# Performance work log

Hardware: AMD Instinct MI355X
Metric: run time of the kernel (lower is better)

Reference implementation:

```python
import jax, jax.numpy as jnp
import numpy as np

RADIUS = 0.1
NSAMPLE = 32


def ball_query_cnt(radius, nsample, xyz, new_xyz):
    """xyz: (B,N,3), new_xyz: (B,npoint,3) -> cnt (B,npoint) int32, idx (B,npoint,nsample) int32.
    Matches pointnet2 CUDA semantics: first `nsample` in-radius points in index order;
    unfilled slots replicate the first found index (0 if none found)."""
    N = xyz.shape[1]
    # (B, npoint, N) squared distances
    d2 = jnp.sum((new_xyz[:, :, None, :] - xyz[:, None, :, :]) ** 2, axis=-1)
    mask = d2 < radius * radius
    pos = jnp.arange(N, dtype=jnp.int32)
    # key encodes position so that top_k returns the LOWEST valid positions first
    key = jnp.where(mask, N - pos, -N)
    topk_vals, _ = jax.lax.top_k(key, nsample)          # (B, npoint, nsample)
    valid = topk_vals > 0
    idx = (N - topk_vals).astype(jnp.int32)
    first = jnp.where(valid[..., :1], idx[..., :1], 0)   # fill value per query
    idx = jnp.where(valid, idx, first)
    cnt = jnp.minimum(mask.sum(axis=-1), nsample).astype(jnp.int32)
    return cnt, idx


def group(features, idx):
    """features: (B,C,N), idx: (B,npoint,nsample) -> (B,C,npoint,nsample)."""
    return jax.vmap(lambda f, i: f[:, i])(features, idx)


def setup_inputs() -> dict:
    key = jax.random.key(0)
    k1, k2, k3 = jax.random.split(key, 3)
    B, N, npoint, C = 4, 16384, 2048, 64
    xyz = jax.random.uniform(k1, (B, N, 3), dtype=jnp.float32)
    new_xyz = jax.random.uniform(k2, (B, npoint, 3), dtype=jnp.float32)
    features = jax.random.normal(k3, (B, C, N), dtype=jnp.float32)
    return {"xyz": xyz, "new_xyz": new_xyz, "features": features}


def reference(xyz, new_xyz, features):
    idx_cnt, idx = ball_query_cnt(RADIUS, NSAMPLE, xyz, new_xyz)
    xyz_t = jnp.transpose(xyz, (0, 2, 1))                      # (B,3,N)
    grouped_xyz = group(xyz_t, idx)                            # (B,3,npoint,nsample)
    grouped_xyz = grouped_xyz - jnp.transpose(new_xyz, (0, 2, 1))[..., None]
    grouped_features = group(features, idx)                    # (B,C,npoint,nsample)
    new_features = jnp.concatenate([grouped_xyz, grouped_features], axis=1)
    return idx_cnt, new_features
```

## Files before the change

### kernel.cpp

```cpp
#include <hip/hip_runtime.h>

#define B        4
#define N        16384
#define NPOINT   2048
#define C        64
#define NSAMPLE  32
#define CH       (C + 3)
#define RADIUS2  0.01f
#define NCELL    1000
#define CSTRIDE  1032
#define CAP      256

#define WAVE_FENCE() asm volatile("s_waitcnt lgkmcnt(0)" ::: "memory")

__device__ __forceinline__ int clamp10(int v) {
    return v < 0 ? 0 : (v > 9 ? 9 : v);
}

__device__ __forceinline__ int cell_of(float x, float y, float z) {
    return (clamp10((int)(x * 10.f)) * 10 + clamp10((int)(y * 10.f))) * 10
         + clamp10((int)(z * 10.f));
}

__global__ __launch_bounds__(256) void zero_kernel(int* __restrict__ p, int n) {
    const int i = blockIdx.x * 256 + threadIdx.x;
    if (i < n) p[i] = 0;
}

__device__ __forceinline__ void transpose_body(const float* __restrict__ f,
                                               float* __restrict__ ft,
                                               int n0, int b, int t,
                                               float (*tile)[65]) {
    const int r16 = t >> 4;
    const int x4  = t & 15;
    #pragma unroll
    for (int it = 0; it < 4; ++it) {
        const int cc = it * 16 + r16;
        const float4 v = *(const float4*)(f + ((size_t)b * C + cc) * N + n0 + x4 * 4);
        tile[cc][x4 * 4 + 0] = v.x;
        tile[cc][x4 * 4 + 1] = v.y;
        tile[cc][x4 * 4 + 2] = v.z;
        tile[cc][x4 * 4 + 3] = v.w;
    }
    __syncthreads();
    #pragma unroll
    for (int it = 0; it < 4; ++it) {
        const int nn = it * 16 + r16;
        float4 v;
        v.x = tile[x4 * 4 + 0][nn];
        v.y = tile[x4 * 4 + 1][nn];
        v.z = tile[x4 * 4 + 2][nn];
        v.w = tile[x4 * 4 + 3][nn];
        *(float4*)(ft + ((size_t)b * N + n0 + nn) * C + x4 * 4) = v;
    }
}

__global__ __launch_bounds__(256) void prep_kernel(const float* __restrict__ xyz,
                                                   int* __restrict__ cnt,
                                                   const float* __restrict__ f,
                                                   float* __restrict__ ft) {
    __shared__ float tile[64][65];
    if (blockIdx.x < (B * N / 256)) {
        const int g = blockIdx.x * 256 + threadIdx.x;
        const int b = g >> 14;
        const float x = xyz[g * 3 + 0], y = xyz[g * 3 + 1], z = xyz[g * 3 + 2];
        atomicAdd(&cnt[(b << 10) + cell_of(x, y, z)], 1);
    } else {
        const int bi = blockIdx.x - (B * N / 256);
        transpose_body(f, ft, (bi & 255) * 64, bi >> 8, threadIdx.x, tile);
    }
}

__global__ __launch_bounds__(256) void feat_transpose_kernel(
    const float* __restrict__ f, float* __restrict__ ft) {
    __shared__ float tile[64][65];
    transpose_body(f, ft, blockIdx.x * 64, blockIdx.y, threadIdx.x, tile);
}

__global__ __launch_bounds__(1024) void prefix_kernel(int* __restrict__ cnt,
                                                      int* __restrict__ cs) {
    __shared__ int wsum[16];
    const int t = threadIdx.x, b = blockIdx.x;
    const int w = t >> 6, l = t & 63;
    const int v = (t < NCELL) ? cnt[(b << 10) + t] : 0;
    int inc = v;
    #pragma unroll
    for (int off = 1; off < 64; off <<= 1) {
        const int u = __shfl_up(inc, off);
        if (l >= off) inc += u;
    }
    if (l == 63) wsum[w] = inc;
    __syncthreads();
    if (t < 16) {
        int s = wsum[t];
        #pragma unroll
        for (int off = 1; off < 16; off <<= 1) {
            const int u = __shfl_up(s, off, 16);
            if (t >= off) s += u;
        }
        wsum[t] = s;
    }
    __syncthreads();
    const int base = (w > 0) ? wsum[w - 1] : 0;
    const int excl = base + inc - v;
    if (t <= NCELL) cs[b * CSTRIDE + t] = excl;
    if (t < NCELL)  cnt[(b << 10) + t] = excl;
}

__global__ __launch_bounds__(256) void scatter_kernel(const float* __restrict__ xyz,
                                                      int* __restrict__ cursor,
                                                      float4* __restrict__ sp) {
    const int g = blockIdx.x * 256 + threadIdx.x;
    const int b = g >> 14;
    const int n = g & (N - 1);
    const float x = xyz[g * 3 + 0], y = xyz[g * 3 + 1], z = xyz[g * 3 + 2];
    const int pos = atomicAdd(&cursor[(b << 10) + cell_of(x, y, z)], 1);
    sp[(b << 14) + pos] = make_float4(x, y, z, __int_as_float(n));
}

__global__ __launch_bounds__(256, 6) void qg_fused_kernel(
    const float*  __restrict__ xyz,
    const float*  __restrict__ new_xyz,
    const float*  __restrict__ ft,
    const int*    __restrict__ cs,
    const float4* __restrict__ sp,
    float* __restrict__ out_cnt,
    float* __restrict__ out_feat)
{
    const int w = threadIdx.x >> 6;
    const int l = threadIdx.x & 63;
    const int q = blockIdx.x * 4 + w;
    const int b = q >> 11;
    const int j = q & (NPOINT - 1);

    __shared__ int   cand_s[4][CAP];
    __shared__ int   si_s[4][NSAMPLE];
    __shared__ float tile_s[4][35 * 33];
    int*   cand = cand_s[w];
    int*   s_i  = si_s[w];
    float* tile = tile_s[w];

    const float qx = new_xyz[q * 3 + 0];
    const float qy = new_xyz[q * 3 + 1];
    const float qz = new_xyz[q * 3 + 2];

    const int cx = clamp10((int)(qx * 10.f));
    const int cy = clamp10((int)(qy * 10.f));
    const int cz = clamp10((int)(qz * 10.f));
    const int z0 = cz > 0 ? cz - 1 : 0;
    const int z1 = cz < 9 ? cz + 1 : 9;

    int sv = 0, ev = 0;
    if (l < 9) {
        const int xx = cx - 1 + l / 3;
        const int yy = cy - 1 + l % 3;
        if (xx >= 0 && xx <= 9 && yy >= 0 && yy <= 9) {
            const int cb = (xx * 10 + yy) * 10;
            sv = cs[b * CSTRIDE + cb + z0];
            ev = cs[b * CSTRIDE + cb + z1 + 1];
        }
    }
    int rs[9], re[9];
    #pragma unroll
    for (int r = 0; r < 9; ++r) {
        rs[r] = __shfl(sv, r);
        re[r] = __shfl(ev, r);
    }

    const unsigned long long ltmask = (1ull << l) - 1ull;
    const float4* spb = sp + ((size_t)b << 14);

    float4 pt[9];
    bool   a[9];
    #pragma unroll
    for (int r = 0; r < 9; ++r) {
        const int p = rs[r] + l;
        a[r] = p < re[r];
        pt[r] = a[r] ? spb[p] : make_float4(1e9f, 1e9f, 1e9f, 0.f);
    }
    int total = 0, ncand = 0;
    #pragma unroll
    for (int r = 0; r < 9; ++r) {
        const float dx = pt[r].x - qx, dy = pt[r].y - qy, dz = pt[r].z - qz;
        const float d2 = dx * dx + dy * dy + dz * dz;
        const bool in = a[r] && (d2 < RADIUS2);
        const unsigned long long m = __ballot(in);
        if (in) {
            const int slot = ncand + __popcll(m & ltmask);
            if (slot < CAP) cand[slot] = __float_as_int(pt[r].w);
        }
        const int c = __popcll(m);
        total += c;
        ncand = ncand + c > CAP ? CAP : ncand + c;
    }
    #pragma unroll 1
    for (int r = 0; r < 9; ++r) {
        #pragma unroll 1
        for (int p0 = rs[r] + 64; p0 < re[r]; p0 += 64) {
            const int p = p0 + l;
            const bool act = p < re[r];
            float4 pv = make_float4(1e9f, 1e9f, 1e9f, 0.f);
            if (act) pv = spb[p];
            const float dx = pv.x - qx, dy = pv.y - qy, dz = pv.z - qz;
            const float d2 = dx * dx + dy * dy + dz * dz;
            const bool in = act && (d2 < RADIUS2);
            const unsigned long long m = __ballot(in);
            if (in) {
                const int slot = ncand + __popcll(m & ltmask);
                if (slot < CAP) cand[slot] = __float_as_int(pv.w);
            }
            const int c = __popcll(m);
            total += c;
            ncand = ncand + c > CAP ? CAP : ncand + c;
        }
    }
    WAVE_FENCE();

    int cntv;
    if (total > CAP) {
        const float* xb = xyz + (size_t)b * N * 3;
        int cnt2 = 0;
        for (int base = 0; base < N; base += 64) {
            const int p = base + l;
            const float dx = xb[p * 3 + 0] - qx;
            const float dy = xb[p * 3 + 1] - qy;
            const float dz = xb[p * 3 + 2] - qz;
            const float d2 = dx * dx + dy * dy + dz * dz;
            const bool in = d2 < RADIUS2;
            const unsigned long long m = __ballot(in);
            if (in) {
                const int slot = cnt2 + __popcll(m & ltmask);
                if (slot < NSAMPLE) s_i[slot] = p;
            }
            cnt2 += __popcll(m);
            if (cnt2 >= NSAMPLE) break;
        }
        cntv = cnt2 < NSAMPLE ? cnt2 : NSAMPLE;
    } else {
        const int K = ncand;
        for (int c = l; c < K; c += 64) {
            const int v = cand[c];
            int rnk = 0;
            for (int i = 0; i < K; ++i) rnk += (cand[i] < v) ? 1 : 0;
            if (rnk < NSAMPLE) s_i[rnk] = v;
        }
        cntv = total < NSAMPLE ? total : NSAMPLE;
    }
    WAVE_FENCE();

    if (l == 0) out_cnt[q] = (float)cntv;
    if (l < NSAMPLE && l >= cntv) s_i[l] = (cntv > 0) ? s_i[0] : 0;
    WAVE_FENCE();

    if (l < NSAMPLE) {
        const int i = s_i[l];
        const float* xp = xyz + ((size_t)b * N + i) * 3;
        tile[0 * 33 + l] = xp[0] - qx;
        tile[1 * 33 + l] = xp[1] - qy;
        tile[2 * 33 + l] = xp[2] - qz;
    }
    const float4* ft4 = (const float4*)ft;
    #pragma unroll
    for (int t = 0; t < 4; ++t) {
        const int k  = t * 8 + (l >> 3);
        const int c4 = l & 7;
        const float4 v = ft4[((size_t)b * N + s_i[k]) * (C / 4) + c4];
        const int ch = 3 + c4 * 4;
        tile[(ch + 0) * 33 + k] = v.x;
        tile[(ch + 1) * 33 + k] = v.y;
        tile[(ch + 2) * 33 + k] = v.z;
        tile[(ch + 3) * 33 + k] = v.w;
    }
    WAVE_FENCE();

    float4* of4 = (float4*)out_feat;
    #pragma unroll
    for (int t = 0; t < 5; ++t) {
        const int e4 = t * 64 + l;
        if (e4 < 35 * 8) {
            const int ch = e4 >> 3;
            const int k4 = e4 & 7;
            float4 v;
            v.x = tile[ch * 33 + k4 * 4 + 0];
            v.y = tile[ch * 33 + k4 * 4 + 1];
            v.z = tile[ch * 33 + k4 * 4 + 2];
            v.w = tile[ch * 33 + k4 * 4 + 3];
            of4[((size_t)(b * CH + ch) * NPOINT + j) * 8 + k4] = v;
        }
    }
    WAVE_FENCE();

    #pragma unroll
    for (int t = 0; t < 4; ++t) {
        const int k  = t * 8 + (l >> 3);
        const int c4 = 8 + (l & 7);
        const float4 v = ft4[((size_t)b * N + s_i[k]) * (C / 4) + c4];
        const int r = (c4 - 8) * 4;
        tile[(r + 0) * 33 + k] = v.x;
        tile[(r + 1) * 33 + k] = v.y;
        tile[(r + 2) * 33 + k] = v.z;
        tile[(r + 3) * 33 + k] = v.w;
    }
    WAVE_FENCE();

    #pragma unroll
    for (int t = 0; t < 4; ++t) {
        const int e4  = t * 64 + l;
        const int chr = e4 >> 3;
        const int k4  = e4 & 7;
        float4 v;
        v.x = tile[chr * 33 + k4 * 4 + 0];
        v.y = tile[chr * 33 + k4 * 4 + 1];
        v.z = tile[chr * 33 + k4 * 4 + 2];
        v.w = tile[chr * 33 + k4 * 4 + 3];
        of4[((size_t)(b * CH + 35 + chr) * NPOINT + j) * 8 + k4] = v;
    }
}

template <bool TRANSPOSED>
__global__ __launch_bounds__(64) void qg_wave_kernel(
    const float* __restrict__ xyz,
    const float* __restrict__ new_xyz,
    const float* __restrict__ feat,
    float* __restrict__ out_cnt,
    float* __restrict__ out_feat)
{
    const int q = blockIdx.x;
    const int b = q >> 11;
    const int j = q & (NPOINT - 1);
    const int l = threadIdx.x;

    __shared__ int   s_idx[NSAMPLE];
    __shared__ float s_tile[CH * 33];

    const float qx = new_xyz[q * 3 + 0];
    const float qy = new_xyz[q * 3 + 1];
    const float qz = new_xyz[q * 3 + 2];
    const float* xb = xyz + (size_t)b * N * 3;

    int cnt = 0;
    for (int base = 0; base < N; base += 64) {
        const int p = base + l;
        const float dx = xb[p * 3 + 0] - qx;
        const float dy = xb[p * 3 + 1] - qy;
        const float dz = xb[p * 3 + 2] - qz;
        const float d2 = dx * dx + dy * dy + dz * dz;
        const bool in = d2 < RADIUS2;
        const unsigned long long m = __ballot(in);
        if (in) {
            const int slot = cnt + __popcll(m & ((1ull << l) - 1ull));
            if (slot < NSAMPLE) s_idx[slot] = p;
        }
        cnt += __popcll(m);
        if (cnt >= NSAMPLE) break;
    }
    if (cnt > NSAMPLE) cnt = NSAMPLE;

    if (l == 0) out_cnt[q] = (float)cnt;
    __syncthreads();
    if (l < NSAMPLE && l >= cnt) s_idx[l] = (cnt > 0) ? s_idx[0] : 0;
    __syncthreads();

    #pragma unroll
    for (int p = 0; p < 8; ++p) {
        const int k  = p * 4 + (l >> 4);
        const int c4 = l & 15;
        const int i  = s_idx[k];
        if (TRANSPOSED) {
            const float4 v = ((const float4*)(feat + ((size_t)b * N + i) * C))[c4];
            const int ch = 3 + c4 * 4;
            s_tile[(ch + 0) * 33 + k] = v.x;
            s_tile[(ch + 1) * 33 + k] = v.y;
            s_tile[(ch + 2) * 33 + k] = v.z;
            s_tile[(ch + 3) * 33 + k] = v.w;
        } else {
            #pragma unroll
            for (int cc2 = 0; cc2 < 4; ++cc2) {
                const int c = c4 * 4 + cc2;
                s_tile[(3 + c) * 33 + k] = feat[((size_t)b * C + c) * N + i];
            }
        }
    }
    if (l < NSAMPLE) {
        const int i = s_idx[l];
        const float* xp = xyz + ((size_t)b * N + i) * 3;
        s_tile[0 * 33 + l] = xp[0] - qx;
        s_tile[1 * 33 + l] = xp[1] - qy;
        s_tile[2 * 33 + l] = xp[2] - qz;
    }
    __syncthreads();

    float4* of4 = (float4*)out_feat;
    for (int e4 = l; e4 < CH * 8; e4 += 64) {
        const int ch = e4 >> 3;
        const int k4 = e4 & 7;
        float4 v;
        v.x = s_tile[ch * 33 + k4 * 4 + 0];
        v.y = s_tile[ch * 33 + k4 * 4 + 1];
        v.z = s_tile[ch * 33 + k4 * 4 + 2];
        v.w = s_tile[ch * 33 + k4 * 4 + 3];
        of4[((size_t)(b * CH + ch) * NPOINT + j) * 8 + k4] = v;
    }
}

extern "C" void kernel_launch(void* const* d_in, const int* in_sizes, int n_in,
                              void* d_out, int out_size, void* d_ws, size_t ws_size,
                              hipStream_t stream) {
    const float* xyz      = (const float*)d_in[0];
    const float* new_xyz  = (const float*)d_in[1];
    const float* features = (const float*)d_in[2];

    float* out_cnt  = (float*)d_out;
    float* out_feat = out_cnt + (size_t)B * NPOINT;

    char* ws = (char*)d_ws;
    const size_t ftB = (size_t)B * N * C * sizeof(float);
    const size_t spB = (size_t)B * N * sizeof(float4);
    const size_t csB = (size_t)B * CSTRIDE * sizeof(int);
    const size_t ccB = (size_t)B * 1024 * sizeof(int);
    const size_t need = ftB + spB + csB + ccB;

    if (ws_size >= need) {
        float*  ft = (float*)ws;
        float4* sp = (float4*)(ws + ftB);
        int*    cs = (int*)(ws + ftB + spB);
        int*    cc = (int*)(ws + ftB + spB + csB);
        zero_kernel<<<(B * 1024 + 255) / 256, 256, 0, stream>>>(cc, B * 1024);
        prep_kernel<<<(B * N / 256) + B * (N / 64), 256, 0, stream>>>(xyz, cc,
                                                                      features, ft);
        prefix_kernel<<<B, 1024, 0, stream>>>(cc, cs);
        scatter_kernel<<<B * N / 256, 256, 0, stream>>>(xyz, cc, sp);
        qg_fused_kernel<<<B * NPOINT / 4, 256, 0, stream>>>(xyz, new_xyz, ft, cs, sp,
                                                            out_cnt, out_feat);
    } else if (ws_size >= ftB) {
        float* ft = (float*)ws;
        feat_transpose_kernel<<<dim3(N / 64, B), 256, 0, stream>>>(features, ft);
        qg_wave_kernel<true><<<B * NPOINT, 64, 0, stream>>>(xyz, new_xyz, ft,
                                                            out_cnt, out_feat);
    } else {
        qg_wave_kernel<false><<<B * NPOINT, 64, 0, stream>>>(xyz, new_xyz, features,
                                                             out_cnt, out_feat);
    }
}
```

Baseline: 136.1 us.

## Fuse prep, prefix, scatter and query-group into one persistent kernel with grid barriers

Replaces the five-kernel pipeline with a zero kernel plus one persistent mega kernel. Inside it, grid-stride loops run the cell counting and feature transpose, the prefix scan, the point scatter and the per-query grouping, separated by atomic-flag grid barriers. The grid is sized from the occupancy query so all blocks stay co-resident. The aim is to remove launch gaps and tail effects between stages, at the cost of spin-wait barriers and lower occupancy during the query phase. The query body also drops its register-prefetched first pass in favour of a single generic loop, which may lose some memory-level parallelism.

```diff
diff --git a/kernel.cpp b/kernel.cpp
--- a/kernel.cpp
+++ b/kernel.cpp
@@ -10,6 +10,7 @@
 #define NCELL    1000
 #define CSTRIDE  1032
 #define CAP      256
+#define NTILE    (B * (N / 64))
 
 #define WAVE_FENCE() asm volatile("s_waitcnt lgkmcnt(0)" ::: "memory")
 
@@ -25,6 +26,23 @@
 __global__ __launch_bounds__(256) void zero_kernel(int* __restrict__ p, int n) {
     const int i = blockIdx.x * 256 + threadIdx.x;
     if (i < n) p[i] = 0;
+}
+
+__device__ __forceinline__ void grid_barrier(int* bar, int ph, int nb) {
+    __syncthreads();
+    if (threadIdx.x == 0) {
+        const int prev = __hip_atomic_fetch_add(bar + ph, 1, __ATOMIC_ACQ_REL,
+                                                __HIP_MEMORY_SCOPE_AGENT);
+        if (prev == nb - 1) {
+            __hip_atomic_store(bar + 4 + ph, 1, __ATOMIC_RELEASE,
+                               __HIP_MEMORY_SCOPE_AGENT);
+        } else {
+            while (!__hip_atomic_load(bar + 4 + ph, __ATOMIC_ACQUIRE,
+                                      __HIP_MEMORY_SCOPE_AGENT))
+                __builtin_amdgcn_s_sleep(2);
+        }
+    }
+    __syncthreads();
 }
 
 __device__ __forceinline__ void transpose_body(const float* __restrict__ f,
@@ -55,90 +73,19 @@
     }
 }
 
-__global__ __launch_bounds__(256) void prep_kernel(const float* __restrict__ xyz,
-                                                   int* __restrict__ cnt,
-                                                   const float* __restrict__ f,
-                                                   float* __restrict__ ft) {
-    __shared__ float tile[64][65];
-    if (blockIdx.x < (B * N / 256)) {
-        const int g = blockIdx.x * 256 + threadIdx.x;
-        const int b = g >> 14;
-        const float x = xyz[g * 3 + 0], y = xyz[g * 3 + 1], z = xyz[g * 3 + 2];
-        atomicAdd(&cnt[(b << 10) + cell_of(x, y, z)], 1);
-    } else {
-        const int bi = blockIdx.x - (B * N / 256);
-        transpose_body(f, ft, (bi & 255) * 64, bi >> 8, threadIdx.x, tile);
-    }
-}
-
-__global__ __launch_bounds__(256) void feat_transpose_kernel(
-    const float* __restrict__ f, float* __restrict__ ft) {
-    __shared__ float tile[64][65];
-    transpose_body(f, ft, blockIdx.x * 64, blockIdx.y, threadIdx.x, tile);
-}
-
-__global__ __launch_bounds__(1024) void prefix_kernel(int* __restrict__ cnt,
-                                                      int* __restrict__ cs) {
-    __shared__ int wsum[16];
-    const int t = threadIdx.x, b = blockIdx.x;
-    const int w = t >> 6, l = t & 63;
-    const int v = (t < NCELL) ? cnt[(b << 10) + t] : 0;
-    int inc = v;
-    #pragma unroll
-    for (int off = 1; off < 64; off <<= 1) {
-        const int u = __shfl_up(inc, off);
-        if (l >= off) inc += u;
-    }
-    if (l == 63) wsum[w] = inc;
-    __syncthreads();
-    if (t < 16) {
-        int s = wsum[t];
-        #pragma unroll
-        for (int off = 1; off < 16; off <<= 1) {
-            const int u = __shfl_up(s, off, 16);
-            if (t >= off) s += u;
-        }
-        wsum[t] = s;
-    }
-    __syncthreads();
-    const int base = (w > 0) ? wsum[w - 1] : 0;
-    const int excl = base + inc - v;
-    if (t <= NCELL) cs[b * CSTRIDE + t] = excl;
-    if (t < NCELL)  cnt[(b << 10) + t] = excl;
-}
-
-__global__ __launch_bounds__(256) void scatter_kernel(const float* __restrict__ xyz,
-                                                      int* __restrict__ cursor,
-                                                      float4* __restrict__ sp) {
-    const int g = blockIdx.x * 256 + threadIdx.x;
-    const int b = g >> 14;
-    const int n = g & (N - 1);
-    const float x = xyz[g * 3 + 0], y = xyz[g * 3 + 1], z = xyz[g * 3 + 2];
-    const int pos = atomicAdd(&cursor[(b << 10) + cell_of(x, y, z)], 1);
-    sp[(b << 14) + pos] = make_float4(x, y, z, __int_as_float(n));
-}
-
-__global__ __launch_bounds__(256, 6) void qg_fused_kernel(
+__device__ __forceinline__ void qg_wave_body(
+    int q, int l,
     const float*  __restrict__ xyz,
     const float*  __restrict__ new_xyz,
     const float*  __restrict__ ft,
     const int*    __restrict__ cs,
     const float4* __restrict__ sp,
+    int* cand, int* s_i, float* tile,
     float* __restrict__ out_cnt,
     float* __restrict__ out_feat)
 {
-    const int w = threadIdx.x >> 6;
-    const int l = threadIdx.x & 63;
-    const int q = blockIdx.x * 4 + w;
     const int b = q >> 11;
     const int j = q & (NPOINT - 1);
-
-    __shared__ int   cand_s[4][CAP];
-    __shared__ int   si_s[4][NSAMPLE];
-    __shared__ float tile_s[4][35 * 33];
-    int*   cand = cand_s[w];
-    int*   s_i  = si_s[w];
-    float* tile = tile_s[w];
 
     const float qx = new_xyz[q * 3 + 0];
     const float qy = new_xyz[q * 3 + 1];
@@ -160,54 +107,24 @@
             ev = cs[b * CSTRIDE + cb + z1 + 1];
         }
     }
-    int rs[9], re[9];
-    #pragma unroll
+
+    const unsigned long long ltmask = (1ull << l) - 1ull;
+    int total = 0, ncand = 0;
     for (int r = 0; r < 9; ++r) {
-        rs[r] = __shfl(sv, r);
-        re[r] = __shfl(ev, r);
-    }
-
-    const unsigned long long ltmask = (1ull << l) - 1ull;
-    const float4* spb = sp + ((size_t)b << 14);
-
-    float4 pt[9];
-    bool   a[9];
-    #pragma unroll
-    for (int r = 0; r < 9; ++r) {
-        const int p = rs[r] + l;
-        a[r] = p < re[r];
-        pt[r] = a[r] ? spb[p] : make_float4(1e9f, 1e9f, 1e9f, 0.f);
-    }
-    int total = 0, ncand = 0;
-    #pragma unroll
-    for (int r = 0; r < 9; ++r) {
-        const float dx = pt[r].x - qx, dy = pt[r].y - qy, dz = pt[r].z - qz;
-        const float d2 = dx * dx + dy * dy + dz * dz;
-        const bool in = a[r] && (d2 < RADIUS2);
-        const unsigned long long m = __ballot(in);
-        if (in) {
-            const int slot = ncand + __popcll(m & ltmask);
-            if (slot < CAP) cand[slot] = __float_as_int(pt[r].w);
-        }
-        const int c = __popcll(m);
-        total += c;
-        ncand = ncand + c > CAP ? CAP : ncand + c;
-    }
-    #pragma unroll 1
-    for (int r = 0; r < 9; ++r) {
-        #pragma unroll 1
-        for (int p0 = rs[r] + 64; p0 < re[r]; p0 += 64) {
+        const int rs = __shfl(sv, r);
+        const int re = __shfl(ev, r);
+        for (int p0 = rs; p0 < re; p0 += 64) {
             const int p = p0 + l;
-            const bool act = p < re[r];
-            float4 pv = make_float4(1e9f, 1e9f, 1e9f, 0.f);
-            if (act) pv = spb[p];
-            const float dx = pv.x - qx, dy = pv.y - qy, dz = pv.z - qz;
+            const bool act = p < re;
+            float4 pt = make_float4(1e9f, 1e9f, 1e9f, 0.f);
+            if (act) pt = sp[(b << 14) + p];
+            const float dx = pt.x - qx, dy = pt.y - qy, dz = pt.z - qz;
             const float d2 = dx * dx + dy * dy + dz * dz;
             const bool in = act && (d2 < RADIUS2);
             const unsigned long long m = __ballot(in);
             if (in) {
                 const int slot = ncand + __popcll(m & ltmask);
-                if (slot < CAP) cand[slot] = __float_as_int(pv.w);
+                if (slot < CAP) cand[slot] = __float_as_int(pt.w);
             }
             const int c = __popcll(m);
             total += c;
@@ -317,6 +234,155 @@
     }
 }
 
+__global__ __launch_bounds__(256, 4) void mega2_kernel(
+    const float*  __restrict__ xyz,
+    const float*  __restrict__ new_xyz,
+    const float*  __restrict__ f,
+    float*        __restrict__ ft,
+    int*          __restrict__ cs,
+    float4*       __restrict__ sp,
+    int*          __restrict__ cc,
+    int*          __restrict__ bar,
+    float*        __restrict__ out_cnt,
+    float*        __restrict__ out_feat)
+{
+    const int nb  = gridDim.x;
+    const int bid = blockIdx.x;
+    const int t   = threadIdx.x;
+
+    __shared__ __align__(16) char smem[23088];
+    __shared__ int wsum[4];
+
+    for (int g = bid * 256 + t; g < B * N; g += nb * 256) {
+        const int b = g >> 14;
+        const float x = xyz[g * 3 + 0], y = xyz[g * 3 + 1], z = xyz[g * 3 + 2];
+        atomicAdd(&cc[(b << 10) + cell_of(x, y, z)], 1);
+    }
+    {
+        float (*tile)[65] = (float (*)[65])smem;
+        for (int ti = bid; ti < NTILE; ti += nb) {
+            transpose_body(f, ft, (ti & 255) * 64, ti >> 8, t, tile);
+            __syncthreads();
+        }
+    }
+    grid_barrier(bar, 0, nb);
+
+    if (bid < B) {
+        const int b = bid;
+        const int4 a = ((const int4*)(cc + (b << 10)))[t];
+        const int s = a.x + a.y + a.z + a.w;
+        const int w = t >> 6, l = t & 63;
+        int inc = s;
+        #pragma unroll
+        for (int off = 1; off < 64; off <<= 1) {
+            const int u = __shfl_up(inc, off);
+            if (l >= off) inc += u;
+        }
+        if (l == 63) wsum[w] = inc;
+        __syncthreads();
+        int wbase = 0;
+        #pragma unroll
+        for (int k = 0; k < 4; ++k) wbase += (k < w) ? wsum[k] : 0;
+        const int e0 = wbase + inc - s;
+        int4 e;
+        e.x = e0; e.y = e0 + a.x; e.z = e.y + a.y; e.w = e.z + a.z;
+        ((int4*)(cs + b * CSTRIDE))[t] = e;
+        ((int4*)(cc + (b << 10)))[t]  = e;
+    }
+    grid_barrier(bar, 1, nb);
+
+    for (int g = bid * 256 + t; g < B * N; g += nb * 256) {
+        const int b = g >> 14, n = g & (N - 1);
+        const float x = xyz[g * 3 + 0], y = xyz[g * 3 + 1], z = xyz[g * 3 + 2];
+        const int pos = atomicAdd(&cc[(b << 10) + cell_of(x, y, z)], 1);
+        sp[(b << 14) + pos] = make_float4(x, y, z, __int_as_float(n));
+    }
+    grid_barrier(bar, 2, nb);
+
+    {
+        const int w = t >> 6, l = t & 63;
+        int*   cand = (int*)smem + w * CAP;
+        int*   s_i  = (int*)smem + 4 * CAP + w * NSAMPLE;
+        float* tile = (float*)smem + 4 * CAP + 4 * NSAMPLE + w * (35 * 33);
+        for (int q = bid * 4 + w; q < B * NPOINT; q += nb * 4) {
+            qg_wave_body(q, l, xyz, new_xyz, ft, cs, sp, cand, s_i, tile,
+                         out_cnt, out_feat);
+            WAVE_FENCE();
+        }
+    }
+}
+
+__global__ __launch_bounds__(256) void count_kernel(const float* __restrict__ xyz,
+                                                    int* __restrict__ cnt) {
+    const int g = blockIdx.x * 256 + threadIdx.x;
+    const int b = g >> 14;
+    const float x = xyz[g * 3 + 0], y = xyz[g * 3 + 1], z = xyz[g * 3 + 2];
+    atomicAdd(&cnt[(b << 10) + cell_of(x, y, z)], 1);
+}
+
+__global__ __launch_bounds__(1024) void prefix_kernel(int* __restrict__ cnt,
+                                                      int* __restrict__ cs) {
+    __shared__ int wsum[16];
+    const int t = threadIdx.x, b = blockIdx.x;
+    const int w = t >> 6, l = t & 63;
+    const int v = (t < NCELL) ? cnt[(b << 10) + t] : 0;
+    int inc = v;
+    #pragma unroll
+    for (int off = 1; off < 64; off <<= 1) {
+        const int u = __shfl_up(inc, off);
+        if (l >= off) inc += u;
+    }
+    if (l == 63) wsum[w] = inc;
+    __syncthreads();
+    if (t < 16) {
+        int s = wsum[t];
+        #pragma unroll
+        for (int off = 1; off < 16; off <<= 1) {
+            const int u = __shfl_up(s, off, 16);
+            if (t >= off) s += u;
+        }
+        wsum[t] = s;
+    }
+    __syncthreads();
+    const int base = (w > 0) ? wsum[w - 1] : 0;
+    const int excl = base + inc - v;
+    if (t <= NCELL) cs[b * CSTRIDE + t] = excl;
+    if (t < NCELL)  cnt[(b << 10) + t] = excl;
+}
+
+__global__ __launch_bounds__(256) void scatter_kernel(const float* __restrict__ xyz,
+                                                      int* __restrict__ cursor,
+                                                      float4* __restrict__ sp) {
+    const int g = blockIdx.x * 256 + threadIdx.x;
+    const int b = g >> 14;
+    const int n = g & (N - 1);
+    const float x = xyz[g * 3 + 0], y = xyz[g * 3 + 1], z = xyz[g * 3 + 2];
+    const int pos = atomicAdd(&cursor[(b << 10) + cell_of(x, y, z)], 1);
+    sp[(b << 14) + pos] = make_float4(x, y, z, __int_as_float(n));
+}
+
+__global__ __launch_bounds__(256) void feat_transpose_kernel(
+    const float* __restrict__ f, float* __restrict__ ft) {
+    __shared__ float tile[64][65];
+    transpose_body(f, ft, blockIdx.x * 64, blockIdx.y, threadIdx.x, tile);
+}
+
+__global__ __launch_bounds__(64) void qg_grid_kernel(
+    const float*  __restrict__ xyz,
+    const float*  __restrict__ new_xyz,
+    const float*  __restrict__ ft,
+    const int*    __restrict__ cs,
+    const float4* __restrict__ sp,
+    float* __restrict__ out_cnt,
+    float* __restrict__ out_feat)
+{
+    __shared__ int   cand[CAP];
+    __shared__ int   s_i[NSAMPLE];
+    __shared__ float tile[35 * 33];
+    qg_wave_body(blockIdx.x, threadIdx.x, xyz, new_xyz, ft, cs, sp,
+                 cand, s_i, tile, out_cnt, out_feat);
+}
+
 template <bool TRANSPOSED>
 __global__ __launch_bounds__(64) void qg_wave_kernel(
     const float* __restrict__ xyz,
@@ -417,21 +483,50 @@
     const size_t ftB = (size_t)B * N * C * sizeof(float);
     const size_t spB = (size_t)B * N * sizeof(float4);
     const size_t csB = (size_t)B * CSTRIDE * sizeof(int);
-    const size_t ccB = (size_t)B * 1024 * sizeof(int);
+    const size_t ccB = (size_t)(B * 1024 + 16) * sizeof(int);
     const size_t need = ftB + spB + csB + ccB;
 
     if (ws_size >= need) {
-        float*  ft = (float*)ws;
-        float4* sp = (float4*)(ws + ftB);
-        int*    cs = (int*)(ws + ftB + spB);
-        int*    cc = (int*)(ws + ftB + spB + csB);
-        zero_kernel<<<(B * 1024 + 255) / 256, 256, 0, stream>>>(cc, B * 1024);
-        prep_kernel<<<(B * N / 256) + B * (N / 64), 256, 0, stream>>>(xyz, cc,
-                                                                      features, ft);
+        float*  ft  = (float*)ws;
+        float4* sp  = (float4*)(ws + ftB);
+        int*    cs  = (int*)(ws + ftB + spB);
+        int*    cc  = (int*)(ws + ftB + spB + csB);
+        int*    bar = cc + B * 1024;
+
+        static int mega_grid = -2;
+        if (mega_grid == -2) {
+            int dev = 0, ncu = 0, occ = 0;
+            hipError_t e0 = hipGetDevice(&dev);
+            hipError_t e1 = hipDeviceGetAttribute(
+                &ncu, hipDeviceAttributeMultiprocessorCount, dev);
+            hipError_t e2 = hipOccupancyMaxActiveBlocksPerMultiprocessor(
+                &occ, mega2_kernel, 256, 0);
+            if (e0 == hipSuccess && e1 == hipSuccess && e2 == hipSuccess &&
+                occ >= 1 && ncu >= 8) {
+                long cap = (long)occ * ncu;
+                mega_grid = cap < NTILE ? (int)cap : NTILE;
+                if (mega_grid < 64) mega_grid = -1;
+            } else {
+                mega_grid = -1;
+            }
+        }
+
+        if (mega_grid > 0) {
+            zero_kernel<<<(B * 1024 + 16 + 255) / 256, 256, 0, stream>>>(
+                cc, B * 1024 + 16);
+            mega2_kernel<<<mega_grid, 256, 0, stream>>>(
+                xyz, new_xyz, features, ft, cs, sp, cc, bar, out_cnt, out_feat);
+            return;
+        }
+
+        zero_kernel<<<(B * 1024 + 16 + 255) / 256, 256, 0, stream>>>(
+            cc, B * 1024 + 16);
+        count_kernel<<<B * N / 256, 256, 0, stream>>>(xyz, cc);
         prefix_kernel<<<B, 1024, 0, stream>>>(cc, cs);
         scatter_kernel<<<B * N / 256, 256, 0, stream>>>(xyz, cc, sp);
-        qg_fused_kernel<<<B * NPOINT / 4, 256, 0, stream>>>(xyz, new_xyz, ft, cs, sp,
-                                                            out_cnt, out_feat);
+        feat_transpose_kernel<<<dim3(N / 64, B), 256, 0, stream>>>(features, ft);
+        qg_grid_kernel<<<B * NPOINT, 64, 0, stream>>>(xyz, new_xyz, ft, cs, sp,
+                                                      out_cnt, out_feat);
     } else if (ws_size >= ftB) {
         float* ft = (float*)ws;
         feat_transpose_kernel<<<dim3(N / 64, B), 256, 0, stream>>>(features, ft);
```

After: 317.2 us. +133.0%, slower.

## Write grouped features straight to global memory and simplify the neighbor-cell scan loop

Applied to the files above, without the earlier changes.

Drops the per-wave LDS transpose tile and has each lane write its gathered feature and xyz values straight to the output with scalar stores. Each wave now writes eight runs of four consecutive floats per channel plane instead of full 128-byte float4 rows. The batched, fully unrolled first-iteration load of all nine cells is folded back into one generic loop over cells. This cuts LDS use, which may raise occupancy, and removes the tile round-trip and fences, but makes output stores less coalesced and loses the overlapped loads across the nine cells.

```diff
diff --git a/kernel.cpp b/kernel.cpp
--- a/kernel.cpp
+++ b/kernel.cpp
@@ -118,7 +118,7 @@
     sp[(b << 14) + pos] = make_float4(x, y, z, __int_as_float(n));
 }
 
-__global__ __launch_bounds__(256, 6) void qg_fused_kernel(
+__global__ __launch_bounds__(256, 6) void qg_v2_kernel(
     const float*  __restrict__ xyz,
     const float*  __restrict__ new_xyz,
     const float*  __restrict__ ft,
@@ -133,12 +133,10 @@
     const int b = q >> 11;
     const int j = q & (NPOINT - 1);
 
-    __shared__ int   cand_s[4][CAP];
-    __shared__ int   si_s[4][NSAMPLE];
-    __shared__ float tile_s[4][35 * 33];
-    int*   cand = cand_s[w];
-    int*   s_i  = si_s[w];
-    float* tile = tile_s[w];
+    __shared__ int cand_s[4][CAP];
+    __shared__ int si_s[4][NSAMPLE];
+    int* cand = cand_s[w];
+    int* s_i  = si_s[w];
 
     const float qx = new_xyz[q * 3 + 0];
     const float qy = new_xyz[q * 3 + 1];
@@ -160,54 +158,24 @@
             ev = cs[b * CSTRIDE + cb + z1 + 1];
         }
     }
-    int rs[9], re[9];
-    #pragma unroll
+
+    const unsigned long long ltmask = (1ull << l) - 1ull;
+    int total = 0, ncand = 0;
     for (int r = 0; r < 9; ++r) {
-        rs[r] = __shfl(sv, r);
-        re[r] = __shfl(ev, r);
-    }
-
-    const unsigned long long ltmask = (1ull << l) - 1ull;
-    const float4* spb = sp + ((size_t)b << 14);
-
-    float4 pt[9];
-    bool   a[9];
-    #pragma unroll
-    for (int r = 0; r < 9; ++r) {
-        const int p = rs[r] + l;
-        a[r] = p < re[r];
-        pt[r] = a[r] ? spb[p] : make_float4(1e9f, 1e9f, 1e9f, 0.f);
-    }
-    int total = 0, ncand = 0;
-    #pragma unroll
-    for (int r = 0; r < 9; ++r) {
-        const float dx = pt[r].x - qx, dy = pt[r].y - qy, dz = pt[r].z - qz;
-        const float d2 = dx * dx + dy * dy + dz * dz;
-        const bool in = a[r] && (d2 < RADIUS2);
-        const unsigned long long m = __ballot(in);
-        if (in) {
-            const int slot = ncand + __popcll(m & ltmask);
-            if (slot < CAP) cand[slot] = __float_as_int(pt[r].w);
-        }
-        const int c = __popcll(m);
-        total += c;
-        ncand = ncand + c > CAP ? CAP : ncand + c;
-    }
-    #pragma unroll 1
-    for (int r = 0; r < 9; ++r) {
-        #pragma unroll 1
-        for (int p0 = rs[r] + 64; p0 < re[r]; p0 += 64) {
+        const int rs = __shfl(sv, r);
+        const int re = __shfl(ev, r);
+        for (int p0 = rs; p0 < re; p0 += 64) {
             const int p = p0 + l;
-            const bool act = p < re[r];
-            float4 pv = make_float4(1e9f, 1e9f, 1e9f, 0.f);
-            if (act) pv = spb[p];
-            const float dx = pv.x - qx, dy = pv.y - qy, dz = pv.z - qz;
+            const bool act = p < re;
+            float4 pt = make_float4(1e9f, 1e9f, 1e9f, 0.f);
+            if (act) pt = sp[(b << 14) + p];
+            const float dx = pt.x - qx, dy = pt.y - qy, dz = pt.z - qz;
             const float d2 = dx * dx + dy * dy + dz * dz;
             const bool in = act && (d2 < RADIUS2);
             const unsigned long long m = __ballot(in);
             if (in) {
                 const int slot = ncand + __popcll(m & ltmask);
-                if (slot < CAP) cand[slot] = __float_as_int(pv.w);
+                if (slot < CAP) cand[slot] = __float_as_int(pt.w);
             }
             const int c = __popcll(m);
             total += c;
@@ -252,68 +220,34 @@
     if (l < NSAMPLE && l >= cntv) s_i[l] = (cntv > 0) ? s_i[0] : 0;
     WAVE_FENCE();
 
+    const size_t plane = (size_t)NPOINT * NSAMPLE;
+    float* ob = out_feat + (size_t)b * CH * plane + (size_t)j * NSAMPLE;
     if (l < NSAMPLE) {
         const int i = s_i[l];
         const float* xp = xyz + ((size_t)b * N + i) * 3;
-        tile[0 * 33 + l] = xp[0] - qx;
-        tile[1 * 33 + l] = xp[1] - qy;
-        tile[2 * 33 + l] = xp[2] - qz;
-    }
+        ob[0 * plane + l] = xp[0] - qx;
+        ob[1 * plane + l] = xp[1] - qy;
+        ob[2 * plane + l] = xp[2] - qz;
+    }
+
     const float4* ft4 = (const float4*)ft;
     #pragma unroll
     for (int t = 0; t < 4; ++t) {
         const int k  = t * 8 + (l >> 3);
         const int c4 = l & 7;
-        const float4 v = ft4[((size_t)b * N + s_i[k]) * (C / 4) + c4];
-        const int ch = 3 + c4 * 4;
-        tile[(ch + 0) * 33 + k] = v.x;
-        tile[(ch + 1) * 33 + k] = v.y;
-        tile[(ch + 2) * 33 + k] = v.z;
-        tile[(ch + 3) * 33 + k] = v.w;
-    }
-    WAVE_FENCE();
-
-    float4* of4 = (float4*)out_feat;
-    #pragma unroll
-    for (int t = 0; t < 5; ++t) {
-        const int e4 = t * 64 + l;
-        if (e4 < 35 * 8) {
-            const int ch = e4 >> 3;
-            const int k4 = e4 & 7;
-            float4 v;
-            v.x = tile[ch * 33 + k4 * 4 + 0];
-            v.y = tile[ch * 33 + k4 * 4 + 1];
-            v.z = tile[ch * 33 + k4 * 4 + 2];
-            v.w = tile[ch * 33 + k4 * 4 + 3];
-            of4[((size_t)(b * CH + ch) * NPOINT + j) * 8 + k4] = v;
-        }
-    }
-    WAVE_FENCE();
-
-    #pragma unroll
-    for (int t = 0; t < 4; ++t) {
-        const int k  = t * 8 + (l >> 3);
-        const int c4 = 8 + (l & 7);
-        const float4 v = ft4[((size_t)b * N + s_i[k]) * (C / 4) + c4];
-        const int r = (c4 - 8) * 4;
-        tile[(r + 0) * 33 + k] = v.x;
-        tile[(r + 1) * 33 + k] = v.y;
-        tile[(r + 2) * 33 + k] = v.z;
-        tile[(r + 3) * 33 + k] = v.w;
-    }
-    WAVE_FENCE();
-
-    #pragma unroll
-    for (int t = 0; t < 4; ++t) {
-        const int e4  = t * 64 + l;
-        const int chr = e4 >> 3;
-        const int k4  = e4 & 7;
-        float4 v;
-        v.x = tile[chr * 33 + k4 * 4 + 0];
-        v.y = tile[chr * 33 + k4 * 4 + 1];
-        v.z = tile[chr * 33 + k4 * 4 + 2];
-        v.w = tile[chr * 33 + k4 * 4 + 3];
-        of4[((size_t)(b * CH + 35 + chr) * NPOINT + j) * 8 + k4] = v;
+        const int i  = s_i[k];
+        const float4 va = ft4[((size_t)b * N + i) * (C / 4) + c4];
+        const float4 vb = ft4[((size_t)b * N + i) * (C / 4) + 8 + c4];
+        float* oa = ob + (size_t)(3 + c4 * 4) * plane + k;
+        oa[0 * plane] = va.x;
+        oa[1 * plane] = va.y;
+        oa[2 * plane] = va.z;
+        oa[3 * plane] = va.w;
+        float* obp = ob + (size_t)(35 + c4 * 4) * plane + k;
+        obp[0 * plane] = vb.x;
+        obp[1 * plane] = vb.y;
+        obp[2 * plane] = vb.z;
+        obp[3 * plane] = vb.w;
     }
 }
 
@@ -430,8 +364,8 @@
                                                                       features, ft);
         prefix_kernel<<<B, 1024, 0, stream>>>(cc, cs);
         scatter_kernel<<<B * N / 256, 256, 0, stream>>>(xyz, cc, sp);
-        qg_fused_kernel<<<B * NPOINT / 4, 256, 0, stream>>>(xyz, new_xyz, ft, cs, sp,
-                                                            out_cnt, out_feat);
+        qg_v2_kernel<<<B * NPOINT / 4, 256, 0, stream>>>(xyz, new_xyz, ft, cs, sp,
+                                                         out_cnt, out_feat);
     } else if (ws_size >= ftB) {
         float* ft = (float*)ws;
         feat_transpose_kernel<<<dim3(N / 64, B), 256, 0, stream>>>(features, ft);
```

After: 127.2 us. 1.07x faster.
